# Performance work log

Measured on AMD Instinct MI355X. Metric: run time of the kernel, lower is better.

Reference implementation:

```python
import jax, jax.numpy as jnp
import numpy as np

HIDDEN = 1024
HEADS = 16
HEAD = HIDDEN // HEADS


def _ternary_weight(key, shape):
    g = jax.random.normal(key, shape, dtype=jnp.float32)
    return jnp.where(jnp.abs(g) < 0.6, 0.0, jnp.sign(g)).astype(jnp.float32)


def setup_inputs() -> dict:
    key = jax.random.key(0)
    ks = jax.random.split(key, 10)
    x = jax.random.normal(ks[0], (2, 2048, HIDDEN), dtype=jnp.float32)
    d = {"x": x}
    names = ["q", "k", "v", "o"]
    for i, n in enumerate(names):
        d[f"w_{n}"] = _ternary_weight(ks[1 + i], (HIDDEN, HIDDEN))
        d[f"s_{n}"] = jnp.float32(0.02)  # per-layer dequant scale
        d[f"b_{n}"] = jax.random.normal(ks[5 + i], (HIDDEN,), dtype=jnp.float32) * 0.02
    return d


def _tlin(x, w, s, b):
    # dequantized ternary linear: x @ (s * w).T + b
    return jnp.einsum("bsh,oh->bso", x, w) * s + b


def reference(x, w_q, s_q, b_q, w_k, s_k, b_k, w_v, s_v, b_v, w_o, s_o, b_o):
    B, S, H = x.shape
    def split_heads(t):
        return t.reshape(B, S, HEADS, HEAD).transpose(0, 2, 1, 3)  # [B, nH, S, hd]
    q = split_heads(_tlin(x, w_q, s_q, b_q))
    k = split_heads(_tlin(x, w_k, s_k, b_k))
    v = split_heads(_tlin(x, w_v, s_v, b_v))
    scores = jnp.einsum("bhqd,bhkd->bhqk", q, k) / jnp.sqrt(jnp.float32(HEAD))
    attn = jax.nn.softmax(scores, axis=-1)
    ctx = jnp.einsum("bhqk,bhkd->bhqd", attn, v)
    ctx = ctx.transpose(0, 2, 1, 3).reshape(B, S, H)
    return _tlin(ctx, w_o, s_o, b_o)
```

## Files before the change

### kernel.cpp

```cpp
#include <hip/hip_runtime.h>
#include <hip/hip_bf16.h>

typedef unsigned short u16;
typedef __bf16 bf16x8 __attribute__((ext_vector_type(8)));
typedef __bf16 bf16x4 __attribute__((ext_vector_type(4)));
typedef float f32x4 __attribute__((ext_vector_type(4)));
typedef unsigned short u16x8 __attribute__((ext_vector_type(8)));

__device__ inline u16 f2bf(float f) {
    union { float f; unsigned u; } v; v.f = f;
    unsigned r = v.u + 0x7fffu + ((v.u >> 16) & 1u);
    return (u16)(r >> 16);
}

__global__ void convert_kernel(const float* __restrict__ x,
                               const float* __restrict__ wq, const float* __restrict__ wk,
                               const float* __restrict__ wv, const float* __restrict__ wo,
                               u16* __restrict__ dst) {
    long g = (long)blockIdx.x * blockDim.x + threadIdx.x;
    const float* src; long base;
    const long GX = 1048576, GW = 262144;
    if (g < GX)            { src = x;  base = 0; }
    else if (g < GX + GW)  { src = wq; base = GX; }
    else if (g < GX + 2*GW){ src = wk; base = GX + GW; }
    else if (g < GX + 3*GW){ src = wv; base = GX + 2*GW; }
    else                   { src = wo; base = GX + 3*GW; }
    long rel = g - base;
    float4 v = reinterpret_cast<const float4*>(src)[rel];
    ushort4 o;
    o.x = f2bf(v.x); o.y = f2bf(v.y); o.z = f2bf(v.z); o.w = f2bf(v.w);
    reinterpret_cast<ushort4*>(dst)[g] = o;
}

__device__ inline void gemm_mainloop(const u16* __restrict__ A, const u16* __restrict__ W,
                                     int t0, int n0, u16* As, u16* Bs, f32x4 acc[4][4]) {
    const int tid = threadIdx.x;
    const int wid = tid >> 6, lane = tid & 63, quad = lane >> 4, ln = lane & 15;
    const int wm = wid >> 1, wn = wid & 1;
#pragma unroll
    for (int im = 0; im < 4; im++)
#pragma unroll
        for (int in = 0; in < 4; in++) acc[im][in] = (f32x4){0.f, 0.f, 0.f, 0.f};

    for (int k0 = 0; k0 < 1024; k0 += 64) {
#pragma unroll
        for (int i = 0; i < 4; i++) {
            int chunk = wid * 4 + i;
            int b = chunk * 1024 + lane * 16;
            int row = b >> 7;
            int cb = (b & 127) ^ ((row & 7) << 4);
            const u16* gA = A + (long)(t0 + row) * 1024 + k0 + (cb >> 1);
            const u16* gB = W + (long)(n0 + row) * 1024 + k0 + (cb >> 1);
            __builtin_amdgcn_global_load_lds((const __attribute__((address_space(1))) void*)gA,
                                             (__attribute__((address_space(3))) void*)(As + chunk * 512),
                                             16, 0, 0);
            __builtin_amdgcn_global_load_lds((const __attribute__((address_space(1))) void*)gB,
                                             (__attribute__((address_space(3))) void*)(Bs + chunk * 512),
                                             16, 0, 0);
        }
        __syncthreads();
#pragma unroll
        for (int ks = 0; ks < 2; ks++) {
            bf16x8 af[4], bfr[4];
#pragma unroll
            for (int im = 0; im < 4; im++) {
                int r = wm * 64 + im * 16 + ln;
                int byt = (r * 128 + ks * 64 + quad * 16) ^ ((r & 7) << 4);
                af[im] = *reinterpret_cast<const bf16x8*>((const char*)As + byt);
            }
#pragma unroll
            for (int in = 0; in < 4; in++) {
                int r = wn * 64 + in * 16 + ln;
                int byt = (r * 128 + ks * 64 + quad * 16) ^ ((r & 7) << 4);
                bfr[in] = *reinterpret_cast<const bf16x8*>((const char*)Bs + byt);
            }
#pragma unroll
            for (int im = 0; im < 4; im++)
#pragma unroll
                for (int in = 0; in < 4; in++)
                    acc[im][in] = __builtin_amdgcn_mfma_f32_16x16x32_bf16(af[im], bfr[in], acc[im][in], 0, 0, 0);
        }
        __syncthreads();
    }
}

__global__ void qkv_gemm(const u16* __restrict__ x_bf,
                         const u16* __restrict__ wq, const u16* __restrict__ wk, const u16* __restrict__ wv,
                         const float* __restrict__ sq, const float* __restrict__ sk, const float* __restrict__ sv,
                         const float* __restrict__ bq, const float* __restrict__ bk, const float* __restrict__ bv,
                         u16* __restrict__ q_ws, u16* __restrict__ k_ws, u16* __restrict__ v_ws) {
    __shared__ __align__(16) u16 As[128 * 64];
    __shared__ __align__(16) u16 Bs[128 * 64];
    const int z = blockIdx.z;
    const u16* W   = (z == 0) ? wq : (z == 1) ? wk : wv;
    const float* sp = (z == 0) ? sq : (z == 1) ? sk : sv;
    const float* bp = (z == 0) ? bq : (z == 1) ? bk : bv;
    u16* dst = (z == 0) ? q_ws : (z == 1) ? k_ws : v_ws;
    const float extra = (z == 0) ? 0.125f * 1.44269504088896f : 1.0f;
    const int t0 = blockIdx.x * 128, n0 = blockIdx.y * 128;

    f32x4 acc[4][4];
    gemm_mainloop(x_bf, W, t0, n0, As, Bs, acc);

    const int tid = threadIdx.x;
    const int wid = tid >> 6, lane = tid & 63, quad = lane >> 4, ln = lane & 15;
    const int wm = wid >> 1, wn = wid & 1;
    const float s = sp[0] * extra;
#pragma unroll
    for (int in = 0; in < 4; in++) {
        int col = n0 + wn * 64 + in * 16 + ln;
        float bias = bp[col] * extra;
        int h = col >> 6, d = col & 63;
#pragma unroll
        for (int im = 0; im < 4; im++) {
            int rbase = t0 + wm * 64 + im * 16 + quad * 4;
#pragma unroll
            for (int j = 0; j < 4; j++) {
                int t = rbase + j;
                int b = t >> 11, ss = t & 2047;
                int bh = b * 16 + h;
                float val = acc[im][in][j] * s + bias;
                long idx = (z < 2) ? ((long)(bh * 2048 + ss) * 64 + d)
                                   : ((long)(bh * 64 + d) * 2048 + ss);
                dst[idx] = f2bf(val);
            }
        }
    }
}

#define LDP 72

__global__ void __launch_bounds__(512)
attn_kernel(const u16* __restrict__ q_ws, const u16* __restrict__ k_ws,
            const u16* __restrict__ v_ws, u16* __restrict__ ctx) {
    __shared__ __align__(16) u16 Kb[2][4096];
    __shared__ __align__(16) u16 Vb[2][4096];
    __shared__ u16 Pt[128 * LDP];

    const int tid = threadIdx.x;
    const int wid = tid >> 6, lane = tid & 63, quad = lane >> 4, ln = lane & 15;
    const int bh = blockIdx.y;
    const int q0 = blockIdx.x * 128;
    const u16* qbase = q_ws + (long)bh * 2048 * 64;
    const u16* kbase = k_ws + (long)bh * 2048 * 64;
    const u16* vbase = v_ws + (long)bh * 64 * 2048;

    const int srow = wid * 8 + (lane >> 3);
    const int sel  = 8 * ((lane & 7) ^ ((lane >> 3) & 7));
    const int xr = (ln & 7) << 4;

    bf16x8 aq[2];
#pragma unroll
    for (int ks = 0; ks < 2; ks++)
        aq[ks] = *reinterpret_cast<const bf16x8*>(
            qbase + (long)(q0 + wid * 16 + ln) * 64 + ks * 32 + quad * 8);

    f32x4 acc_o[4];
    float lsum = 0.f;
#pragma unroll
    for (int dt = 0; dt < 4; dt++) acc_o[dt] = (f32x4){0.f, 0.f, 0.f, 0.f};

    const u16* kp = kbase + (long)srow * 64 + sel;
    const u16* vp = vbase + (long)srow * 2048 + sel;

    __builtin_amdgcn_global_load_lds((const __attribute__((address_space(1))) void*)kp,
                                     (__attribute__((address_space(3))) void*)(&Kb[0][wid * 512]),
                                     16, 0, 0);
    __builtin_amdgcn_global_load_lds((const __attribute__((address_space(1))) void*)vp,
                                     (__attribute__((address_space(3))) void*)(&Vb[0][wid * 512]),
                                     16, 0, 0);
    kp += 4096; vp += 64;
    __syncthreads();

    int cur = 0;
    for (int kt = 0; kt < 2048; kt += 64) {
        if (kt + 64 < 2048) {
            __builtin_amdgcn_global_load_lds((const __attribute__((address_space(1))) void*)kp,
                                             (__attribute__((address_space(3))) void*)(&Kb[cur ^ 1][wid * 512]),
                                             16, 0, 0);
            __builtin_amdgcn_global_load_lds((const __attribute__((address_space(1))) void*)vp,
                                             (__attribute__((address_space(3))) void*)(&Vb[cur ^ 1][wid * 512]),
                                             16, 0, 0);
            kp += 4096; vp += 64;
        }
        const char* Kc = (const char*)(&Kb[cur][0]);
        const char* Vc = (const char*)(&Vb[cur][0]);

#pragma unroll
        for (int k8 = 0; k8 < 4; k8++) {
            bf16x8 a0 = *reinterpret_cast<const bf16x8*>(
                Kc + (k8 * 16 + ln) * 128 + ((quad * 16) ^ xr));
            bf16x8 a1 = *reinterpret_cast<const bf16x8*>(
                Kc + (k8 * 16 + ln) * 128 + ((64 + quad * 16) ^ xr));
            f32x4 t = (f32x4){0.f, 0.f, 0.f, 0.f};
            __builtin_amdgcn_s_setprio(1);
            t = __builtin_amdgcn_mfma_f32_16x16x32_bf16(a0, aq[0], t, 0, 0, 0);
            t = __builtin_amdgcn_mfma_f32_16x16x32_bf16(a1, aq[1], t, 0, 0, 0);
            __builtin_amdgcn_s_setprio(0);
            __bf16 p0 = (__bf16)__builtin_amdgcn_exp2f(t[0]);
            __bf16 p1 = (__bf16)__builtin_amdgcn_exp2f(t[1]);
            __bf16 p2 = (__bf16)__builtin_amdgcn_exp2f(t[2]);
            __bf16 p3 = (__bf16)__builtin_amdgcn_exp2f(t[3]);
            lsum += (float)p0 + (float)p1 + (float)p2 + (float)p3;
            *reinterpret_cast<bf16x4*>(Pt + (wid * 16 + ln) * LDP + k8 * 16 + quad * 4)
                = (bf16x4){p0, p1, p2, p3};
        }

#pragma unroll
        for (int step = 0; step < 2; step++) {
            bf16x8 ap = *reinterpret_cast<const bf16x8*>(
                Pt + (wid * 16 + ln) * LDP + step * 32 + quad * 8);
            bf16x8 bv0 = *reinterpret_cast<const bf16x8*>(
                Vc + (0 * 16 + ln) * 128 + ((step * 64 + quad * 16) ^ xr));
            bf16x8 bv1 = *reinterpret_cast<const bf16x8*>(
                Vc + (1 * 16 + ln) * 128 + ((step * 64 + quad * 16) ^ xr));
            bf16x8 bv2 = *reinterpret_cast<const bf16x8*>(
                Vc + (2 * 16 + ln) * 128 + ((step * 64 + quad * 16) ^ xr));
            bf16x8 bv3 = *reinterpret_cast<const bf16x8*>(
                Vc + (3 * 16 + ln) * 128 + ((step * 64 + quad * 16) ^ xr));
            __builtin_amdgcn_s_setprio(1);
            acc_o[0] = __builtin_amdgcn_mfma_f32_16x16x32_bf16(ap, bv0, acc_o[0], 0, 0, 0);
            acc_o[1] = __builtin_amdgcn_mfma_f32_16x16x32_bf16(ap, bv1, acc_o[1], 0, 0, 0);
            acc_o[2] = __builtin_amdgcn_mfma_f32_16x16x32_bf16(ap, bv2, acc_o[2], 0, 0, 0);
            acc_o[3] = __builtin_amdgcn_mfma_f32_16x16x32_bf16(ap, bv3, acc_o[3], 0, 0, 0);
            __builtin_amdgcn_s_setprio(0);
        }
        __syncthreads();
        cur ^= 1;
    }

    const int b = bh >> 4, h = bh & 15;
    float lt = lsum;
    lt += __shfl_xor(lt, 16, 64);
    lt += __shfl_xor(lt, 32, 64);
#pragma unroll
    for (int j = 0; j < 4; j++) {
        float rinv = 1.0f / __shfl(lt, quad * 4 + j, 64);
        int t = b * 2048 + q0 + wid * 16 + quad * 4 + j;
#pragma unroll
        for (int dt = 0; dt < 4; dt++) {
            float val = acc_o[dt][j] * rinv;
            ctx[(long)t * 1024 + h * 64 + dt * 16 + ln] = f2bf(val);
        }
    }
}

__global__ void o_gemm(const u16* __restrict__ ctx, const u16* __restrict__ wo,
                       const float* __restrict__ so, const float* __restrict__ bo,
                       float* __restrict__ out) {
    __shared__ __align__(16) u16 As[128 * 64];
    __shared__ __align__(16) u16 Bs[128 * 64];
    const int t0 = blockIdx.x * 128, n0 = blockIdx.y * 128;
    f32x4 acc[4][4];
    gemm_mainloop(ctx, wo, t0, n0, As, Bs, acc);

    const int tid = threadIdx.x;
    const int wid = tid >> 6, lane = tid & 63, quad = lane >> 4, ln = lane & 15;
    const int wm = wid >> 1, wn = wid & 1;
    const float s = so[0];
#pragma unroll
    for (int in = 0; in < 4; in++) {
        int col = n0 + wn * 64 + in * 16 + ln;
        float bias = bo[col];
#pragma unroll
        for (int im = 0; im < 4; im++) {
            int rbase = t0 + wm * 64 + im * 16 + quad * 4;
#pragma unroll
            for (int j = 0; j < 4; j++)
                out[(long)(rbase + j) * 1024 + col] = acc[im][in][j] * s + bias;
        }
    }
}

extern "C" void kernel_launch(void* const* d_in, const int* in_sizes, int n_in,
                              void* d_out, int out_size, void* d_ws, size_t ws_size,
                              hipStream_t stream) {
    const float* x   = (const float*)d_in[0];
    const float* w_q = (const float*)d_in[1];
    const float* s_q = (const float*)d_in[2];
    const float* b_q = (const float*)d_in[3];
    const float* w_k = (const float*)d_in[4];
    const float* s_k = (const float*)d_in[5];
    const float* b_k = (const float*)d_in[6];
    const float* w_v = (const float*)d_in[7];
    const float* s_v = (const float*)d_in[8];
    const float* b_v = (const float*)d_in[9];
    const float* w_o = (const float*)d_in[10];
    const float* s_o = (const float*)d_in[11];
    const float* b_o = (const float*)d_in[12];

    if (ws_size < (size_t)50331648) return;

    u16* ws     = (u16*)d_ws;
    u16* x_bf   = ws;
    u16* wq_bf  = x_bf  + 4194304;
    u16* wk_bf  = wq_bf + 1048576;
    u16* wv_bf  = wk_bf + 1048576;
    u16* wo_bf  = wv_bf + 1048576;
    u16* q_ws   = wo_bf + 1048576;
    u16* k_ws   = q_ws  + 4194304;
    u16* v_ws   = k_ws  + 4194304;
    u16* ctx_ws = v_ws  + 4194304;

    convert_kernel<<<dim3(8192), dim3(256), 0, stream>>>(x, w_q, w_k, w_v, w_o, ws);
    qkv_gemm<<<dim3(32, 8, 3), dim3(256), 0, stream>>>(x_bf, wq_bf, wk_bf, wv_bf,
                                                       s_q, s_k, s_v, b_q, b_k, b_v,
                                                       q_ws, k_ws, v_ws);
    attn_kernel<<<dim3(16, 32), dim3(512), 0, stream>>>(q_ws, k_ws, v_ws, ctx_ws);
    o_gemm<<<dim3(32, 8), dim3(256), 0, stream>>>(ctx_ws, wo_bf, s_o, b_o, (float*)d_out);
}
```

Measured before the change: 204.0 us.

## Compute softmax row sums via MFMA and rewrite o_gemm with 512-thread double-buffered LDS

In attention, the per-lane scalar sum of exp values followed by cross-lane shuffles is replaced by an extra MFMA of P against a vector of ones. The row sums then land directly in the accumulator layout. The output projection GEMM now uses 512 threads with 8 waves (4x4 by 2 tiles each), double-buffered swizzled LDS staged by global_load_lds, and split A/B loading across wave halves. These changes aim to cut VALU and shuffle work and to overlap loads with MFMA, at the cost of doubled LDS and one extra MFMA per step.

```diff
diff --git a/kernel.cpp b/kernel.cpp
--- a/kernel.cpp
+++ b/kernel.cpp
@@ -155,8 +155,12 @@
         aq[ks] = *reinterpret_cast<const bf16x8*>(
             qbase + (long)(q0 + wid * 16 + ln) * 64 + ks * 32 + quad * 8);
 
+    bf16x8 vones;
+#pragma unroll
+    for (int i = 0; i < 8; i++) vones[i] = (__bf16)1.0f;
+
     f32x4 acc_o[4];
-    float lsum = 0.f;
+    f32x4 acc_l = (f32x4){0.f, 0.f, 0.f, 0.f};
 #pragma unroll
     for (int dt = 0; dt < 4; dt++) acc_o[dt] = (f32x4){0.f, 0.f, 0.f, 0.f};
 
@@ -201,7 +205,6 @@
             __bf16 p1 = (__bf16)__builtin_amdgcn_exp2f(t[1]);
             __bf16 p2 = (__bf16)__builtin_amdgcn_exp2f(t[2]);
             __bf16 p3 = (__bf16)__builtin_amdgcn_exp2f(t[3]);
-            lsum += (float)p0 + (float)p1 + (float)p2 + (float)p3;
             *reinterpret_cast<bf16x4*>(Pt + (wid * 16 + ln) * LDP + k8 * 16 + quad * 4)
                 = (bf16x4){p0, p1, p2, p3};
         }
@@ -223,6 +226,7 @@
             acc_o[1] = __builtin_amdgcn_mfma_f32_16x16x32_bf16(ap, bv1, acc_o[1], 0, 0, 0);
             acc_o[2] = __builtin_amdgcn_mfma_f32_16x16x32_bf16(ap, bv2, acc_o[2], 0, 0, 0);
             acc_o[3] = __builtin_amdgcn_mfma_f32_16x16x32_bf16(ap, bv3, acc_o[3], 0, 0, 0);
+            acc_l    = __builtin_amdgcn_mfma_f32_16x16x32_bf16(ap, vones, acc_l, 0, 0, 0);
             __builtin_amdgcn_s_setprio(0);
         }
         __syncthreads();
@@ -230,12 +234,9 @@
     }
 
     const int b = bh >> 4, h = bh & 15;
-    float lt = lsum;
-    lt += __shfl_xor(lt, 16, 64);
-    lt += __shfl_xor(lt, 32, 64);
 #pragma unroll
     for (int j = 0; j < 4; j++) {
-        float rinv = 1.0f / __shfl(lt, quad * 4 + j, 64);
+        float rinv = 1.0f / acc_l[j];
         int t = b * 2048 + q0 + wid * 16 + quad * 4 + j;
 #pragma unroll
         for (int dt = 0; dt < 4; dt++) {
@@ -245,22 +246,82 @@
     }
 }
 
-__global__ void o_gemm(const u16* __restrict__ ctx, const u16* __restrict__ wo,
-                       const float* __restrict__ so, const float* __restrict__ bo,
-                       float* __restrict__ out) {
-    __shared__ __align__(16) u16 As[128 * 64];
-    __shared__ __align__(16) u16 Bs[128 * 64];
-    const int t0 = blockIdx.x * 128, n0 = blockIdx.y * 128;
-    f32x4 acc[4][4];
-    gemm_mainloop(ctx, wo, t0, n0, As, Bs, acc);
-
+__global__ void __launch_bounds__(512)
+o_gemm(const u16* __restrict__ ctx, const u16* __restrict__ wo,
+       const float* __restrict__ so, const float* __restrict__ bo,
+       float* __restrict__ out) {
+    __shared__ __align__(16) u16 As[2][128 * 64];
+    __shared__ __align__(16) u16 Bs[2][128 * 64];
     const int tid = threadIdx.x;
     const int wid = tid >> 6, lane = tid & 63, quad = lane >> 4, ln = lane & 15;
-    const int wm = wid >> 1, wn = wid & 1;
+    const int wm = wid >> 2, wn = wid & 3;
+    const int t0 = blockIdx.x * 128, n0 = blockIdx.y * 128;
+
+    const bool stA = (wid < 4);
+    const u16* gbase = stA ? ctx : wo;
+    const int r0 = stA ? t0 : n0;
+    const int cbase = (wid & 3) * 4;
+
+    f32x4 acc[4][2];
+#pragma unroll
+    for (int im = 0; im < 4; im++)
+#pragma unroll
+        for (int in = 0; in < 2; in++) acc[im][in] = (f32x4){0.f, 0.f, 0.f, 0.f};
+
+    const int sb   = cbase * 1024 + lane * 16;
+    const int srow = sb >> 7;
+    const int scb  = (sb & 127) ^ ((srow & 7) << 4);
+
+#define O_STAGE(buf, k0)                                                              \
+    {                                                                                 \
+        const u16* g = gbase + (long)(r0 + srow) * 1024 + (k0) + (scb >> 1);          \
+        u16* d = (stA ? &As[buf][0] : &Bs[buf][0]) + cbase * 512;                     \
+        _Pragma("unroll")                                                             \
+        for (int i = 0; i < 4; i++) {                                                 \
+            __builtin_amdgcn_global_load_lds(                                         \
+                (const __attribute__((address_space(1))) void*)(g + (long)i * 8 * 1024), \
+                (__attribute__((address_space(3))) void*)(d + i * 512), 16, 0, 0);    \
+        }                                                                             \
+    }
+
+    O_STAGE(0, 0);
+    __syncthreads();
+
+    int cur = 0;
+    for (int k0 = 0; k0 < 1024; k0 += 64) {
+        if (k0 + 64 < 1024) O_STAGE(cur ^ 1, k0 + 64);
+        const char* Ac = (const char*)&As[cur][0];
+        const char* Bc = (const char*)&Bs[cur][0];
+#pragma unroll
+        for (int ks = 0; ks < 2; ks++) {
+            bf16x8 af[4], bfr[2];
+#pragma unroll
+            for (int im = 0; im < 4; im++) {
+                int r = wm * 64 + im * 16 + ln;
+                int byt = (r * 128 + ks * 64 + quad * 16) ^ ((r & 7) << 4);
+                af[im] = *reinterpret_cast<const bf16x8*>(Ac + byt);
+            }
+#pragma unroll
+            for (int in = 0; in < 2; in++) {
+                int r = wn * 32 + in * 16 + ln;
+                int byt = (r * 128 + ks * 64 + quad * 16) ^ ((r & 7) << 4);
+                bfr[in] = *reinterpret_cast<const bf16x8*>(Bc + byt);
+            }
+#pragma unroll
+            for (int im = 0; im < 4; im++)
+#pragma unroll
+                for (int in = 0; in < 2; in++)
+                    acc[im][in] = __builtin_amdgcn_mfma_f32_16x16x32_bf16(af[im], bfr[in], acc[im][in], 0, 0, 0);
+        }
+        __syncthreads();
+        cur ^= 1;
+    }
+#undef O_STAGE
+
     const float s = so[0];
 #pragma unroll
-    for (int in = 0; in < 4; in++) {
-        int col = n0 + wn * 64 + in * 16 + ln;
+    for (int in = 0; in < 2; in++) {
+        int col = n0 + wn * 32 + in * 16 + ln;
         float bias = bo[col];
 #pragma unroll
         for (int im = 0; im < 4; im++) {
@@ -307,5 +368,5 @@
                                                        s_q, s_k, s_v, b_q, b_k, b_v,
                                                        q_ws, k_ws, v_ws);
     attn_kernel<<<dim3(16, 32), dim3(512), 0, stream>>>(q_ws, k_ws, v_ws, ctx_ws);
-    o_gemm<<<dim3(32, 8), dim3(256), 0, stream>>>(ctx_ws, wo_bf, s_o, b_o, (float*)d_out);
-}
+    o_gemm<<<dim3(32, 8), dim3(512), 0, stream>>>(ctx_ws, wo_bf, s_o, b_o, (float*)d_out);
+}
```

After: 192.8 us. -5.4%, faster.
